# Performance work log

Measured on AMD Instinct MI355X. Metric: run time of the kernel, lower is better.

Reference implementation:

```python
import jax, jax.numpy as jnp
import numpy as np

WH, WW = 7, 7
N = WH * WW
DIM = 384
HEADS = 12
NW = 64          # windows per image
B_ = 2048        # batch * NW


def _relative_position_index():
    ch, cw = np.meshgrid(np.arange(WH), np.arange(WW), indexing='ij')
    coords = np.stack([ch, cw]).reshape(2, -1)                      # [2, N]
    rel = coords[:, :, None] - coords[:, None, :]                   # [2, N, N]
    rel = rel.transpose(1, 2, 0)
    rel[:, :, 0] += WH - 1
    rel[:, :, 1] += WW - 1
    rel[:, :, 0] *= 2 * WW - 1
    return jnp.asarray(rel.sum(-1), dtype=jnp.int32)                # [N, N]


def setup_inputs() -> dict:
    key = jax.random.key(0)
    ks = jax.random.split(key, 7)
    return {
        'x': jax.random.normal(ks[0], (B_, N, DIM), dtype=jnp.float32),
        'qkv_w': jax.random.normal(ks[1], (3 * DIM, DIM), dtype=jnp.float32) * 0.02,
        'qkv_b': jax.random.normal(ks[2], (3 * DIM,), dtype=jnp.float32) * 0.02,
        'proj_w': jax.random.normal(ks[3], (DIM, DIM), dtype=jnp.float32) * 0.02,
        'proj_b': jax.random.normal(ks[4], (DIM,), dtype=jnp.float32) * 0.02,
        'bias_table': jax.random.normal(ks[5], ((2 * WH - 1) * (2 * WW - 1), HEADS), dtype=jnp.float32) * 0.02,
        'mask': jax.random.normal(ks[6], (NW, N, N), dtype=jnp.float32),
        'rel_idx': _relative_position_index(),
    }


def reference(x, qkv_w, qkv_b, proj_w, proj_b, bias_table, mask, rel_idx):
    B_, n, C = x.shape
    H = HEADS
    hd = C // H
    scale = hd ** (-0.5)

    qkv = x @ qkv_w.T + qkv_b                                        # [B_, N, 3C]
    qkv = qkv.reshape(B_, n, 3, H, hd).transpose(2, 0, 3, 1, 4)      # [3, B_, H, N, hd]
    q, k, v = qkv[0], qkv[1], qkv[2]

    attn = jnp.einsum('bhqd,bhkd->bhqk', q * scale, k)               # [B_, H, N, N]

    rpb = bias_table[rel_idx.reshape(-1)].reshape(n, n, H)           # gather [N, N, H]
    attn = attn + rpb.transpose(2, 0, 1)[None]                       # [B_, H, N, N]

    nW = mask.shape[0]
    attn = attn.reshape(B_ // nW, nW, H, n, n) + mask[None, :, None]
    attn = attn.reshape(B_, H, n, n)
    attn = jax.nn.softmax(attn, axis=-1)

    out = jnp.einsum('bhqk,bhkd->bhqd', attn, v)                     # [B_, H, N, hd]
    out = out.transpose(0, 2, 1, 3).reshape(B_, n, C)
    return out @ proj_w.T + proj_b
```

## Files before the change

kernel.cpp:

```cpp
#include <hip/hip_runtime.h>
#include <hip/hip_bf16.h>
#include <cstdint>
#include <cstddef>

#define NTOK 49
#define DIM 384
#define HEADS 12
#define HD 32
#define NWIN 64
#define BATCH 2048
#define MROWS (BATCH * NTOK)

typedef unsigned short u16;
typedef __bf16 bf16x8 __attribute__((ext_vector_type(8)));
typedef unsigned short u16x8 __attribute__((ext_vector_type(8)));
typedef float f32x4 __attribute__((ext_vector_type(4)));

__device__ __forceinline__ u16 f2b(float f) {
  union { float f; unsigned u; } v; v.f = f;
  unsigned r = v.u + 0x7fffu + ((v.u >> 16) & 1u);
  return (u16)(r >> 16);
}

__device__ __forceinline__ bf16x8 ld_bf8(const u16* p) {
  u16x8 u = *(const u16x8*)p;
  return __builtin_bit_cast(bf16x8, u);
}

__device__ __forceinline__ void gload_lds16(const void* g, void* l) {
  __builtin_amdgcn_global_load_lds(
      (const __attribute__((address_space(1))) unsigned*)g,
      (__attribute__((address_space(3))) unsigned*)l, 16, 0, 0);
}

__global__ __launch_bounds__(256) void k_cast(const float* __restrict__ in,
                                              u16* __restrict__ out, int n4) {
  int i = blockIdx.x * 256 + threadIdx.x;
  if (i < n4) {
    float4 v = ((const float4*)in)[i];
    ushort4 o;
    o.x = f2b(v.x); o.y = f2b(v.y); o.z = f2b(v.z); o.w = f2b(v.w);
    ((ushort4*)out)[i] = o;
  }
}

__global__ __launch_bounds__(256) void k_rpbm(const float* __restrict__ bias_table,
                                              const float* __restrict__ mask,
                                              const int* __restrict__ rel_idx,
                                              float* __restrict__ out) {
  int idx = blockIdx.x * 256 + threadIdx.x;
  int r  = idx & 3;
  int l  = (idx >> 2) & 63;
  int ni = (idx >> 8) & 3;
  int mi = (idx >> 10) & 3;
  int w  = (idx >> 12) & 63;
  int h  = idx >> 18;
  int row = mi * 16 + (l >> 4) * 4 + r;
  int col = ni * 16 + (l & 15);
  float v = -1e30f;
  if (row < NTOK && col < NTOK)
    v = bias_table[rel_idx[row * NTOK + col] * HEADS + h] +
        mask[(w * NTOK + row) * NTOK + col];
  out[idx] = v;
}

template <int OUT_BF16>
__global__ __launch_bounds__(256) void k_gemm(const u16* __restrict__ A,
                                              const u16* __restrict__ B,
                                              const float* __restrict__ bias,
                                              void* __restrict__ Cv,
                                              int K, int N, int ntn, int grid_div8) {
  __shared__ u16 As[128 * 32];
  __shared__ u16 Bs[128 * 32];
  int bid = blockIdx.x;
  int tile = (bid & 7) * grid_div8 + (bid >> 3);
  int mt = tile / ntn, nt = tile % ntn;
  long m0 = (long)mt * 128;
  int n0 = nt * 128;
  int tid = threadIdx.x;
  int lane = tid & 63, wid = tid >> 6;
  int wr = (wid >> 1) * 64, wc = (wid & 1) * 64;
  int c = lane & 15, g = lane >> 4;

  int srow = wid * 16 + (lane >> 2);
  int scol = (lane & 3) * 8;
  const u16* gA = A + (m0 + srow) * (long)K + scol;
  const u16* gB = B + (long)(n0 + srow) * K + scol;
  u16* lA = &As[srow * 32 + scol];
  u16* lB = &Bs[srow * 32 + scol];

  f32x4 acc[4][4] = {};
  for (int kt = 0; kt < K; kt += 32) {
    __syncthreads();
    gload_lds16(gA + kt, lA);
    gload_lds16(gA + kt + 64L * K, lA + 64 * 32);
    gload_lds16(gB + kt, lB);
    gload_lds16(gB + kt + 64L * K, lB + 64 * 32);
    __syncthreads();
    bf16x8 af[4], bf_[4];
#pragma unroll
    for (int i = 0; i < 4; ++i) {
      af[i]  = ld_bf8(&As[(wr + i * 16 + c) * 32 + g * 8]);
      bf_[i] = ld_bf8(&Bs[(wc + i * 16 + c) * 32 + g * 8]);
    }
#pragma unroll
    for (int mi = 0; mi < 4; ++mi)
#pragma unroll
      for (int ni = 0; ni < 4; ++ni)
        acc[mi][ni] = __builtin_amdgcn_mfma_f32_16x16x32_bf16(
            af[mi], bf_[ni], acc[mi][ni], 0, 0, 0);
  }

#pragma unroll
  for (int mi = 0; mi < 4; ++mi)
#pragma unroll
    for (int ni = 0; ni < 4; ++ni) {
      int colg = n0 + wc + ni * 16 + c;
      float bv = bias[colg];
#pragma unroll
      for (int r = 0; r < 4; ++r) {
        long rowg = m0 + wr + mi * 16 + g * 4 + r;
        float val = acc[mi][ni][r] + bv;
        if (OUT_BF16)
          ((u16*)Cv)[rowg * N + colg] = f2b(val);
        else
          ((float*)Cv)[rowg * N + colg] = val;
      }
    }
}

__global__ __launch_bounds__(256) void k_attn(const u16* __restrict__ qkv,
                                              const float* __restrict__ rpbm,
                                              u16* __restrict__ attnout) {
  __shared__ u16 P_lds[4][64 * 64];
  __shared__ u16 vT_lds[4][32 * 64];
  int lane = threadIdx.x & 63, wid = threadIdx.x >> 6;
  int task = blockIdx.x * 4 + wid;
  int b = task / 12, h = task - b * 12;
  int w = b & 63;
  const u16* base = qkv + (size_t)b * (NTOK * 1152);
  int c = lane & 15, g = lane >> 4;

  u16* vt = vT_lds[wid];
  {
    const u16* vbase = base + 2 * DIM + h * HD;
#pragma unroll
    for (int t = 0; t < 4; ++t) {
      int idx = t * 64 + lane;
      int j = idx >> 2, d0 = (idx & 3) * 8;
      int jr = j < NTOK ? j : NTOK - 1;
      u16x8 vv = *(const u16x8*)(vbase + (size_t)jr * 1152 + d0);
#pragma unroll
      for (int dd = 0; dd < 8; ++dd) {
        int d = d0 + dd;
        int byte = (d * 128 + j * 2) ^ ((d & 7) << 4);
        *(u16*)((char*)vt + byte) = (u16)vv[dd];
      }
    }
  }

  bf16x8 qa[4], kb[4];
#pragma unroll
  for (int mi = 0; mi < 4; ++mi) {
    int row = mi * 16 + c; if (row > NTOK - 1) row = NTOK - 1;
    qa[mi] = ld_bf8(base + (size_t)row * 1152 + h * HD + g * 8);
  }
#pragma unroll
  for (int ni = 0; ni < 4; ++ni) {
    int row = ni * 16 + c; if (row > NTOK - 1) row = NTOK - 1;
    kb[ni] = ld_bf8(base + (size_t)row * 1152 + DIM + h * HD + g * 8);
  }

  f32x4 s[4][4] = {};
#pragma unroll
  for (int mi = 0; mi < 4; ++mi)
#pragma unroll
    for (int ni = 0; ni < 4; ++ni)
      s[mi][ni] = __builtin_amdgcn_mfma_f32_16x16x32_bf16(qa[mi], kb[ni],
                                                          s[mi][ni], 0, 0, 0);

  const float scale = 0.17677669529663687f;
  const f32x4* rp = (const f32x4*)(rpbm + ((size_t)(h * 64 + w)) * 4096);
#pragma unroll
  for (int mi = 0; mi < 4; ++mi)
#pragma unroll
    for (int ni = 0; ni < 4; ++ni) {
      f32x4 rv = rp[(mi * 4 + ni) * 64 + lane];
#pragma unroll
      for (int r = 0; r < 4; ++r)
        s[mi][ni][r] = s[mi][ni][r] * scale + rv[r];
    }

#pragma unroll
  for (int mi = 0; mi < 4; ++mi)
#pragma unroll
    for (int r = 0; r < 4; ++r) {
      float mx = fmaxf(fmaxf(s[mi][0][r], s[mi][1][r]),
                       fmaxf(s[mi][2][r], s[mi][3][r]));
      mx = fmaxf(mx, __shfl_xor(mx, 1));
      mx = fmaxf(mx, __shfl_xor(mx, 2));
      mx = fmaxf(mx, __shfl_xor(mx, 4));
      mx = fmaxf(mx, __shfl_xor(mx, 8));
      float sum = 0.f;
#pragma unroll
      for (int ni = 0; ni < 4; ++ni) {
        float p = __expf(s[mi][ni][r] - mx);
        s[mi][ni][r] = p;
        sum += p;
      }
      sum += __shfl_xor(sum, 1);
      sum += __shfl_xor(sum, 2);
      sum += __shfl_xor(sum, 4);
      sum += __shfl_xor(sum, 8);
      float inv = __builtin_amdgcn_rcpf(sum);
#pragma unroll
      for (int ni = 0; ni < 4; ++ni) s[mi][ni][r] *= inv;
    }

  u16* pl = P_lds[wid];
#pragma unroll
  for (int mi = 0; mi < 4; ++mi)
#pragma unroll
    for (int ni = 0; ni < 4; ++ni) {
      int col = ni * 16 + c;
#pragma unroll
      for (int r = 0; r < 4; ++r) {
        int row = mi * 16 + g * 4 + r;
        int byte = (row * 128 + col * 2) ^ ((row & 7) << 4);
        *(u16*)((char*)pl + byte) = f2b(s[mi][ni][r]);
      }
    }
  asm volatile("s_waitcnt lgkmcnt(0)" ::: "memory");

  f32x4 o[4][2] = {};
#pragma unroll
  for (int ks = 0; ks < 2; ++ks) {
    bf16x8 vb[2];
#pragma unroll
    for (int n2 = 0; n2 < 2; ++n2) {
      int d = n2 * 16 + c;
      int byte = (d * 128 + ks * 64 + g * 16) ^ ((d & 7) << 4);
      vb[n2] = __builtin_bit_cast(bf16x8, *(const u16x8*)((const char*)vt + byte));
    }
#pragma unroll
    for (int mi = 0; mi < 4; ++mi) {
      int row = mi * 16 + c;
      int byte = (row * 128 + ks * 64 + g * 16) ^ ((row & 7) << 4);
      bf16x8 pa = __builtin_bit_cast(bf16x8, *(const u16x8*)((const char*)pl + byte));
#pragma unroll
      for (int n2 = 0; n2 < 2; ++n2)
        o[mi][n2] = __builtin_amdgcn_mfma_f32_16x16x32_bf16(pa, vb[n2],
                                                            o[mi][n2], 0, 0, 0);
    }
  }

  u16* obase = attnout + (size_t)b * (NTOK * DIM) + h * HD;
#pragma unroll
  for (int mi = 0; mi < 4; ++mi)
#pragma unroll
    for (int r = 0; r < 4; ++r) {
      int row = mi * 16 + g * 4 + r;
      if (row < NTOK) {
#pragma unroll
        for (int n2 = 0; n2 < 2; ++n2)
          obase[(size_t)row * DIM + n2 * 16 + c] = f2b(o[mi][n2][r]);
      }
    }
}

extern "C" void kernel_launch(void* const* d_in, const int* in_sizes, int n_in,
                              void* d_out, int out_size, void* d_ws, size_t ws_size,
                              hipStream_t stream) {
  const float* x       = (const float*)d_in[0];
  const float* qkv_w   = (const float*)d_in[1];
  const float* qkv_b   = (const float*)d_in[2];
  const float* proj_w  = (const float*)d_in[3];
  const float* proj_b  = (const float*)d_in[4];
  const float* bias_tb = (const float*)d_in[5];
  const float* mask    = (const float*)d_in[6];
  const int*   rel_idx = (const int*)d_in[7];
  float* out = (float*)d_out;

  char* ws = (char*)d_ws;
  u16*   xb      = (u16*)(ws + 0);
  u16*   wqkvb   = (u16*)(ws + 77070336);
  u16*   wprojb  = (u16*)(ws + 77955072);
  float* rpbm    = (float*)(ws + 78249984);
  u16*   qkv     = (u16*)(ws + 90832896);
  u16*   attnout = (u16*)(ws + 322043904);

  k_cast<<<37632, 256, 0, stream>>>(x, xb, MROWS * DIM / 4);
  k_cast<<<432, 256, 0, stream>>>(qkv_w, wqkvb, 3 * DIM * DIM / 4);
  k_cast<<<144, 256, 0, stream>>>(proj_w, wprojb, DIM * DIM / 4);

  k_rpbm<<<12288, 256, 0, stream>>>(bias_tb, mask, rel_idx, rpbm);

  k_gemm<1><<<7056, 256, 0, stream>>>(xb, wqkvb, qkv_b, qkv, DIM, 3 * DIM, 9, 882);

  k_attn<<<6144, 256, 0, stream>>>(qkv, rpbm, attnout);

  k_gemm<0><<<2352, 256, 0, stream>>>(attnout, wprojb, proj_b, out, DIM, DIM, 3, 294);

  (void)in_sizes; (void)n_in; (void)out_size; (void)ws_size;
}
```

Measured before the change: 381.8 us.

## Fuse x cast into QKV GEMM, double-buffer GEMM, stage epilogue via LDS

```diff
diff --git a/kernel.cpp b/kernel.cpp
--- a/kernel.cpp
+++ b/kernel.cpp
@@ -5,9 +5,9 @@
 
 #define NTOK 49
 #define DIM 384
+#define KDIM 384
 #define HEADS 12
 #define HD 32
-#define NWIN 64
 #define BATCH 2048
 #define MROWS (BATCH * NTOK)
 
@@ -64,17 +64,15 @@
   out[idx] = v;
 }
 
-template <int OUT_BF16>
-__global__ __launch_bounds__(256) void k_gemm(const u16* __restrict__ A,
+template <int OUT_BF16, int A_F32, int NCOLS, int NTN, int GD8>
+__global__ __launch_bounds__(256) void k_gemm(const void* __restrict__ Av,
                                               const u16* __restrict__ B,
                                               const float* __restrict__ bias,
-                                              void* __restrict__ Cv,
-                                              int K, int N, int ntn, int grid_div8) {
-  __shared__ u16 As[128 * 32];
-  __shared__ u16 Bs[128 * 32];
+                                              void* __restrict__ Cv) {
+  __shared__ u16 sh[16384];
   int bid = blockIdx.x;
-  int tile = (bid & 7) * grid_div8 + (bid >> 3);
-  int mt = tile / ntn, nt = tile % ntn;
+  int tile = (bid & 7) * GD8 + (bid >> 3);
+  int mt = tile / NTN, nt = tile - mt * NTN;
   long m0 = (long)mt * 128;
   int n0 = nt * 128;
   int tid = threadIdx.x;
@@ -84,49 +82,121 @@
 
   int srow = wid * 16 + (lane >> 2);
   int scol = (lane & 3) * 8;
-  const u16* gA = A + (m0 + srow) * (long)K + scol;
-  const u16* gB = B + (long)(n0 + srow) * K + scol;
-  u16* lA = &As[srow * 32 + scol];
-  u16* lB = &Bs[srow * 32 + scol];
+  const u16* gB = B + (long)(n0 + srow) * KDIM + scol;
+
+  const u16* gA16 = nullptr;
+  const float* gAf = nullptr;
+  float4 areg[4];
+  int arow = tid >> 3;
+  int acol = (tid & 7) * 4;
+  if (A_F32) {
+    gAf = (const float*)Av + (m0 + arow) * KDIM + acol;
+#pragma unroll
+    for (int rp = 0; rp < 4; ++rp)
+      areg[rp] = *(const float4*)(gAf + rp * 32 * KDIM);
+  } else {
+    gA16 = (const u16*)Av + (m0 + srow) * (long)KDIM + scol;
+  }
 
   f32x4 acc[4][4] = {};
-  for (int kt = 0; kt < K; kt += 32) {
-    __syncthreads();
-    gload_lds16(gA + kt, lA);
-    gload_lds16(gA + kt + 64L * K, lA + 64 * 32);
-    gload_lds16(gB + kt, lB);
-    gload_lds16(gB + kt + 64L * K, lB + 64 * 32);
-    __syncthreads();
-    bf16x8 af[4], bf_[4];
+
+  auto STAGE = [&](int buf, int ktS) {
+    u16* As = sh + buf * 8192;
+    u16* Bs = As + 4096;
+    if (A_F32) {
+#pragma unroll
+      for (int rp = 0; rp < 4; ++rp) {
+        float4 v = areg[rp];
+        ushort4 o; o.x = f2b(v.x); o.y = f2b(v.y); o.z = f2b(v.z); o.w = f2b(v.w);
+        *(ushort4*)&As[(rp * 32 + arow) * 32 + acol] = o;
+      }
+      if (ktS + 32 < KDIM) {
+#pragma unroll
+        for (int rp = 0; rp < 4; ++rp)
+          areg[rp] = *(const float4*)(gAf + rp * 32 * KDIM + (ktS + 32));
+      }
+    } else {
+      gload_lds16(gA16 + ktS, &((u16*)As)[srow * 32 + scol]);
+      gload_lds16(gA16 + ktS + 64L * KDIM, &((u16*)As)[(srow + 64) * 32 + scol]);
+    }
+    gload_lds16(gB + ktS, &Bs[srow * 32 + scol]);
+    gload_lds16(gB + ktS + 64L * KDIM, &Bs[(srow + 64) * 32 + scol]);
+  };
+
+  STAGE(0, 0);
+  __syncthreads();
+  int cur = 0;
+  for (int kt = 0; kt < KDIM; kt += 32) {
+    if (kt + 32 < KDIM) STAGE(cur ^ 1, kt + 32);
+    const u16* As = sh + cur * 8192;
+    const u16* Bs = As + 4096;
+    bf16x8 af[4], bfr[4];
 #pragma unroll
     for (int i = 0; i < 4; ++i) {
       af[i]  = ld_bf8(&As[(wr + i * 16 + c) * 32 + g * 8]);
-      bf_[i] = ld_bf8(&Bs[(wc + i * 16 + c) * 32 + g * 8]);
+      bfr[i] = ld_bf8(&Bs[(wc + i * 16 + c) * 32 + g * 8]);
     }
 #pragma unroll
     for (int mi = 0; mi < 4; ++mi)
 #pragma unroll
       for (int ni = 0; ni < 4; ++ni)
         acc[mi][ni] = __builtin_amdgcn_mfma_f32_16x16x32_bf16(
-            af[mi], bf_[ni], acc[mi][ni], 0, 0, 0);
-  }
-
-#pragma unroll
-  for (int mi = 0; mi < 4; ++mi)
-#pragma unroll
-    for (int ni = 0; ni < 4; ++ni) {
-      int colg = n0 + wc + ni * 16 + c;
-      float bv = bias[colg];
-#pragma unroll
-      for (int r = 0; r < 4; ++r) {
-        long rowg = m0 + wr + mi * 16 + g * 4 + r;
-        float val = acc[mi][ni][r] + bv;
-        if (OUT_BF16)
-          ((u16*)Cv)[rowg * N + colg] = f2b(val);
-        else
-          ((float*)Cv)[rowg * N + colg] = val;
-      }
-    }
+            af[mi], bfr[ni], acc[mi][ni], 0, 0, 0);
+    __syncthreads();
+    cur ^= 1;
+  }
+
+  if (OUT_BF16) {
+    u16* C = (u16*)Cv;
+#pragma unroll
+    for (int mi = 0; mi < 4; ++mi)
+#pragma unroll
+      for (int ni = 0; ni < 4; ++ni) {
+        int col = wc + ni * 16 + c;
+        float bv = bias[n0 + col];
+#pragma unroll
+        for (int r = 0; r < 4; ++r) {
+          int row = wr + mi * 16 + g * 4 + r;
+          sh[row * 128 + col] = f2b(acc[mi][ni][r] + bv);
+        }
+      }
+    __syncthreads();
+#pragma unroll
+    for (int rep = 0; rep < 8; ++rep) {
+      int idx = rep * 2048 + tid * 8;
+      int row = idx >> 7, col = idx & 127;
+      *(u16x8*)(C + (m0 + row) * NCOLS + n0 + col) = *(const u16x8*)&sh[idx];
+    }
+  } else {
+    float* C = (float*)Cv;
+    float* shf = (float*)sh;
+#pragma unroll
+    for (int chunk = 0; chunk < 2; ++chunk) {
+      __syncthreads();
+      if ((wr >> 6) == chunk) {
+#pragma unroll
+        for (int mi = 0; mi < 4; ++mi)
+#pragma unroll
+          for (int ni = 0; ni < 4; ++ni) {
+            int col = wc + ni * 16 + c;
+            float bv = bias[n0 + col];
+#pragma unroll
+            for (int r = 0; r < 4; ++r) {
+              int lrow = mi * 16 + g * 4 + r;
+              shf[lrow * 128 + col] = acc[mi][ni][r] + bv;
+            }
+          }
+      }
+      __syncthreads();
+#pragma unroll
+      for (int rep = 0; rep < 8; ++rep) {
+        int idx = rep * 1024 + tid * 4;
+        int row = idx >> 7, col = idx & 127;
+        *(float4*)(C + (m0 + chunk * 64 + row) * NCOLS + n0 + col) =
+            *(const float4*)&shf[idx];
+      }
+    }
+  }
 }
 
 __global__ __launch_bounds__(256) void k_attn(const u16* __restrict__ qkv,
@@ -135,9 +205,13 @@
   __shared__ u16 P_lds[4][64 * 64];
   __shared__ u16 vT_lds[4][32 * 64];
   int lane = threadIdx.x & 63, wid = threadIdx.x >> 6;
-  int task = blockIdx.x * 4 + wid;
-  int b = task / 12, h = task - b * 12;
-  int w = b & 63;
+  int blk = blockIdx.x;
+  int w = blk / 96;
+  int rr = blk - w * 96;
+  int j = rr / 3;
+  int hb = rr - j * 3;
+  int b = j * 64 + w;
+  int h = hb * 4 + wid;
   const u16* base = qkv + (size_t)b * (NTOK * 1152);
   int c = lane & 15, g = lane >> 4;
 
@@ -147,13 +221,13 @@
 #pragma unroll
     for (int t = 0; t < 4; ++t) {
       int idx = t * 64 + lane;
-      int j = idx >> 2, d0 = (idx & 3) * 8;
-      int jr = j < NTOK ? j : NTOK - 1;
+      int jj = idx >> 2, d0 = (idx & 3) * 8;
+      int jr = jj < NTOK ? jj : NTOK - 1;
       u16x8 vv = *(const u16x8*)(vbase + (size_t)jr * 1152 + d0);
 #pragma unroll
       for (int dd = 0; dd < 8; ++dd) {
         int d = d0 + dd;
-        int byte = (d * 128 + j * 2) ^ ((d & 7) << 4);
+        int byte = (d * 128 + jj * 2) ^ ((d & 7) << 4);
         *(u16*)((char*)vt + byte) = (u16)vv[dd];
       }
     }
@@ -282,24 +356,24 @@
   float* out = (float*)d_out;
 
   char* ws = (char*)d_ws;
-  u16*   xb      = (u16*)(ws + 0);
-  u16*   wqkvb   = (u16*)(ws + 77070336);
-  u16*   wprojb  = (u16*)(ws + 77955072);
-  float* rpbm    = (float*)(ws + 78249984);
-  u16*   qkv     = (u16*)(ws + 90832896);
-  u16*   attnout = (u16*)(ws + 322043904);
-
-  k_cast<<<37632, 256, 0, stream>>>(x, xb, MROWS * DIM / 4);
+  u16*   wqkvb   = (u16*)(ws + 0);
+  u16*   wprojb  = (u16*)(ws + 884736);
+  float* rpbm    = (float*)(ws + 1179648);
+  u16*   qkv     = (u16*)(ws + 13762560);
+  u16*   attnout = (u16*)(ws + 244973568);
+
   k_cast<<<432, 256, 0, stream>>>(qkv_w, wqkvb, 3 * DIM * DIM / 4);
   k_cast<<<144, 256, 0, stream>>>(proj_w, wprojb, DIM * DIM / 4);
 
   k_rpbm<<<12288, 256, 0, stream>>>(bias_tb, mask, rel_idx, rpbm);
 
-  k_gemm<1><<<7056, 256, 0, stream>>>(xb, wqkvb, qkv_b, qkv, DIM, 3 * DIM, 9, 882);
+  k_gemm<1, 1, 1152, 9, 882><<<7056, 256, 0, stream>>>(
+      (const void*)x, wqkvb, qkv_b, (void*)qkv);
 
   k_attn<<<6144, 256, 0, stream>>>(qkv, rpbm, attnout);
 
-  k_gemm<0><<<2352, 256, 0, stream>>>(attnout, wprojb, proj_b, out, DIM, DIM, 3, 294);
+  k_gemm<0, 0, 384, 3, 294><<<2352, 256, 0, stream>>>(
+      (const void*)attnout, wprojb, proj_b, (void*)out);
 
   (void)in_sizes; (void)n_in; (void)out_size; (void)ws_size;
 }
```

Result: no change. 377.1 us (-1.2%).

## Fuse QKV projection, window attention and output projection into one per-window kernel

Applied to the files above, without the earlier changes.

```diff
diff --git a/kernel.cpp b/kernel.cpp
--- a/kernel.cpp
+++ b/kernel.cpp
@@ -7,9 +7,7 @@
 #define DIM 384
 #define HEADS 12
 #define HD 32
-#define NWIN 64
 #define BATCH 2048
-#define MROWS (BATCH * NTOK)
 
 typedef unsigned short u16;
 typedef __bf16 bf16x8 __attribute__((ext_vector_type(8)));
@@ -27,245 +25,276 @@
   return __builtin_bit_cast(bf16x8, u);
 }
 
-__device__ __forceinline__ void gload_lds16(const void* g, void* l) {
-  __builtin_amdgcn_global_load_lds(
-      (const __attribute__((address_space(1))) unsigned*)g,
-      (__attribute__((address_space(3))) unsigned*)l, 16, 0, 0);
-}
-
-__global__ __launch_bounds__(256) void k_cast(const float* __restrict__ in,
-                                              u16* __restrict__ out, int n4) {
-  int i = blockIdx.x * 256 + threadIdx.x;
-  if (i < n4) {
+#define MFMA16(a, b, cacc) __builtin_amdgcn_mfma_f32_16x16x32_bf16(a, b, cacc, 0, 0, 0)
+
+__global__ __launch_bounds__(256) void k_prep(const float* __restrict__ qkv_w,
+                                              u16* __restrict__ wqkvb,
+                                              const float* __restrict__ proj_w,
+                                              u16* __restrict__ wprojb,
+                                              const float* __restrict__ bias_table,
+                                              const float* __restrict__ mask,
+                                              const int* __restrict__ rel_idx,
+                                              float* __restrict__ rpbm) {
+  int blk = blockIdx.x;
+  if (blk < 576) {
+    const float* in;
+    u16* out;
+    int i;
+    if (blk < 432) { in = qkv_w; out = wqkvb; i = blk * 256 + threadIdx.x; }
+    else           { in = proj_w; out = wprojb; i = (blk - 432) * 256 + threadIdx.x; }
     float4 v = ((const float4*)in)[i];
     ushort4 o;
     o.x = f2b(v.x); o.y = f2b(v.y); o.z = f2b(v.z); o.w = f2b(v.w);
     ((ushort4*)out)[i] = o;
+  } else {
+    int idx = (blk - 576) * 256 + threadIdx.x;
+    int r  = idx & 3;
+    int l  = (idx >> 2) & 63;
+    int ni = (idx >> 8) & 3;
+    int mi = (idx >> 10) & 3;
+    int w  = (idx >> 12) & 63;
+    int h  = idx >> 18;
+    int row = mi * 16 + (l >> 4) * 4 + r;
+    int col = ni * 16 + (l & 15);
+    float v = -1e30f;
+    if (row < NTOK && col < NTOK)
+      v = bias_table[rel_idx[row * NTOK + col] * HEADS + h] +
+          mask[(w * NTOK + row) * NTOK + col];
+    rpbm[idx] = v;
   }
 }
 
-__global__ __launch_bounds__(256) void k_rpbm(const float* __restrict__ bias_table,
-                                              const float* __restrict__ mask,
-                                              const int* __restrict__ rel_idx,
-                                              float* __restrict__ out) {
-  int idx = blockIdx.x * 256 + threadIdx.x;
-  int r  = idx & 3;
-  int l  = (idx >> 2) & 63;
-  int ni = (idx >> 8) & 3;
-  int mi = (idx >> 10) & 3;
-  int w  = (idx >> 12) & 63;
-  int h  = idx >> 18;
-  int row = mi * 16 + (l >> 4) * 4 + r;
-  int col = ni * 16 + (l & 15);
-  float v = -1e30f;
-  if (row < NTOK && col < NTOK)
-    v = bias_table[rel_idx[row * NTOK + col] * HEADS + h] +
-        mask[(w * NTOK + row) * NTOK + col];
-  out[idx] = v;
-}
-
-template <int OUT_BF16>
-__global__ __launch_bounds__(256) void k_gemm(const u16* __restrict__ A,
-                                              const u16* __restrict__ B,
-                                              const float* __restrict__ bias,
-                                              void* __restrict__ Cv,
-                                              int K, int N, int ntn, int grid_div8) {
-  __shared__ u16 As[128 * 32];
-  __shared__ u16 Bs[128 * 32];
-  int bid = blockIdx.x;
-  int tile = (bid & 7) * grid_div8 + (bid >> 3);
-  int mt = tile / ntn, nt = tile % ntn;
-  long m0 = (long)mt * 128;
-  int n0 = nt * 128;
-  int tid = threadIdx.x;
-  int lane = tid & 63, wid = tid >> 6;
-  int wr = (wid >> 1) * 64, wc = (wid & 1) * 64;
-  int c = lane & 15, g = lane >> 4;
-
-  int srow = wid * 16 + (lane >> 2);
-  int scol = (lane & 3) * 8;
-  const u16* gA = A + (m0 + srow) * (long)K + scol;
-  const u16* gB = B + (long)(n0 + srow) * K + scol;
-  u16* lA = &As[srow * 32 + scol];
-  u16* lB = &Bs[srow * 32 + scol];
-
-  f32x4 acc[4][4] = {};
-  for (int kt = 0; kt < K; kt += 32) {
-    __syncthreads();
-    gload_lds16(gA + kt, lA);
-    gload_lds16(gA + kt + 64L * K, lA + 64 * 32);
-    gload_lds16(gB + kt, lB);
-    gload_lds16(gB + kt + 64L * K, lB + 64 * 32);
-    __syncthreads();
-    bf16x8 af[4], bf_[4];
-#pragma unroll
-    for (int i = 0; i < 4; ++i) {
-      af[i]  = ld_bf8(&As[(wr + i * 16 + c) * 32 + g * 8]);
-      bf_[i] = ld_bf8(&Bs[(wc + i * 16 + c) * 32 + g * 8]);
-    }
+__global__ __launch_bounds__(256, 1) void k_fused(const float* __restrict__ x,
+                                                  const u16* __restrict__ wqkv,
+                                                  const float* __restrict__ qkv_b,
+                                                  const u16* __restrict__ wproj,
+                                                  const float* __restrict__ proj_b,
+                                                  const float* __restrict__ rpbm,
+                                                  float* __restrict__ out) {
+  __shared__ __attribute__((aligned(16))) char lds[161792];
+  const int b = blockIdx.x;
+  const int w = b & 63;
+  const int tid = threadIdx.x;
+  const int lane = tid & 63, wid = tid >> 6;
+  const int c = lane & 15, g = lane >> 4;
+  char* xs = lds;
+  char* Ob = lds + 50176;
+  char* wv = lds + 100352 + wid * 15360;
+
+  {
+    const float4* xp = (const float4*)(x + (size_t)b * (NTOK * DIM));
+    for (int i = tid; i < 4704; i += 256) {
+      float4 v = xp[i];
+      int row = i / 96, col4 = i - row * 96;
+      ushort4 o;
+      o.x = f2b(v.x); o.y = f2b(v.y); o.z = f2b(v.z); o.w = f2b(v.w);
+      *(ushort4*)(xs + row * 784 + col4 * 8) = o;
+    }
+    uint4 z = {0, 0, 0, 0};
+    for (int t = tid; t < 735; t += 256)
+      *(uint4*)(xs + 38416 + t * 16) = z;
+  }
+  __syncthreads();
+
+  const float scale = 0.17677669529663687f;
+
+#define LOAD_AB(af, bf, kt, ABASE, ASTRIDE, BPTR)                               \
+  _Pragma("unroll") for (int mi = 0; mi < 4; ++mi)                              \
+      af[mi] = ld_bf8((const u16*)((ABASE) + (mi * 16 + c) * (ASTRIDE)) +       \
+                      (kt) * 32 + g * 8);                                       \
+  _Pragma("unroll") for (int nj = 0; nj < 6; ++nj)                              \
+      bf[nj] = ld_bf8(BPTR[nj] + (kt) * 32);
+
+#define MFMA_46(af, bf, ACC)                                                    \
+  _Pragma("unroll") for (int mi = 0; mi < 4; ++mi)                              \
+  _Pragma("unroll") for (int nj = 0; nj < 6; ++nj)                              \
+      ACC[mi][nj] = MFMA16(af[mi], bf[nj], ACC[mi][nj]);
+
+  for (int hh = 0; hh < 3; ++hh) {
+    const int h = wid * 3 + hh;
+
+    int ncol[6];
+    ncol[0] = h * 32;        ncol[1] = h * 32 + 16;
+    ncol[2] = 384 + h * 32;  ncol[3] = 384 + h * 32 + 16;
+    ncol[4] = 768 + h * 32;  ncol[5] = 768 + h * 32 + 16;
+    const u16* bp[6];
+#pragma unroll
+    for (int nj = 0; nj < 6; ++nj)
+      bp[nj] = wqkv + (size_t)(ncol[nj] + c) * 384 + g * 8;
+
+    f32x4 acc[4][6] = {};
+    {
+      bf16x8 afA[4], bfA[6], afB[4], bfB[6];
+      LOAD_AB(afA, bfA, 0, xs, 784, bp);
+#pragma unroll
+      for (int kt = 0; kt < 12; kt += 2) {
+        if (kt + 1 < 12) { LOAD_AB(afB, bfB, kt + 1, xs, 784, bp); }
+        MFMA_46(afA, bfA, acc);
+        if (kt + 2 < 12) { LOAD_AB(afA, bfA, kt + 2, xs, 784, bp); }
+        MFMA_46(afB, bfB, acc);
+      }
+    }
+
+    asm volatile("s_waitcnt lgkmcnt(0)" ::: "memory");
+    __builtin_amdgcn_sched_barrier(0);
+
+#pragma unroll
+    for (int nj = 0; nj < 6; ++nj) {
+      float bv = qkv_b[ncol[nj] + c];
+      int d = (nj & 1) * 16 + c;
+#pragma unroll
+      for (int mi = 0; mi < 4; ++mi) {
+#pragma unroll
+        for (int r = 0; r < 4; ++r) {
+          int tok = mi * 16 + g * 4 + r;
+          float v = acc[mi][nj][r] + bv;
+          if (nj < 2)
+            *(u16*)(wv + tok * 80 + d * 2) = f2b(v * scale);
+          else if (nj < 4)
+            *(u16*)(wv + 5120 + tok * 80 + d * 2) = f2b(v);
+          else
+            *(u16*)(wv + 10240 + d * 144 + tok * 2) = f2b(v);
+        }
+      }
+    }
+    asm volatile("s_waitcnt lgkmcnt(0)" ::: "memory");
+    __builtin_amdgcn_sched_barrier(0);
+
+    f32x4 s[4][4];
+    {
+      bf16x8 qf[4], kf[4];
+#pragma unroll
+      for (int i = 0; i < 4; ++i) {
+        qf[i] = ld_bf8((const u16*)(wv + (i * 16 + c) * 80) + g * 8);
+        kf[i] = ld_bf8((const u16*)(wv + 5120 + (i * 16 + c) * 80) + g * 8);
+      }
+      f32x4 zf = {0.f, 0.f, 0.f, 0.f};
+#pragma unroll
+      for (int mi = 0; mi < 4; ++mi)
+#pragma unroll
+        for (int nj = 0; nj < 4; ++nj)
+          s[mi][nj] = MFMA16(qf[mi], kf[nj], zf);
+    }
+
+    const f32x4* rp = (const f32x4*)(rpbm + ((size_t)(h * 64 + w)) * 4096);
 #pragma unroll
     for (int mi = 0; mi < 4; ++mi)
 #pragma unroll
-      for (int ni = 0; ni < 4; ++ni)
-        acc[mi][ni] = __builtin_amdgcn_mfma_f32_16x16x32_bf16(
-            af[mi], bf_[ni], acc[mi][ni], 0, 0, 0);
+      for (int nj = 0; nj < 4; ++nj) {
+        f32x4 rv = rp[(mi * 4 + nj) * 64 + lane];
+#pragma unroll
+        for (int r = 0; r < 4; ++r) s[mi][nj][r] += rv[r];
+      }
+
+#pragma unroll
+    for (int mi = 0; mi < 4; ++mi)
+#pragma unroll
+      for (int r = 0; r < 4; ++r) {
+        float mx = fmaxf(fmaxf(s[mi][0][r], s[mi][1][r]),
+                         fmaxf(s[mi][2][r], s[mi][3][r]));
+        mx = fmaxf(mx, __shfl_xor(mx, 1));
+        mx = fmaxf(mx, __shfl_xor(mx, 2));
+        mx = fmaxf(mx, __shfl_xor(mx, 4));
+        mx = fmaxf(mx, __shfl_xor(mx, 8));
+        float sum = 0.f;
+#pragma unroll
+        for (int nj = 0; nj < 4; ++nj) {
+          float p = __expf(s[mi][nj][r] - mx);
+          s[mi][nj][r] = p;
+          sum += p;
+        }
+        sum += __shfl_xor(sum, 1);
+        sum += __shfl_xor(sum, 2);
+        sum += __shfl_xor(sum, 4);
+        sum += __shfl_xor(sum, 8);
+        float inv = __builtin_amdgcn_rcpf(sum);
+#pragma unroll
+        for (int nj = 0; nj < 4; ++nj) s[mi][nj][r] *= inv;
+      }
+
+#pragma unroll
+    for (int mi = 0; mi < 4; ++mi)
+#pragma unroll
+      for (int nj = 0; nj < 4; ++nj) {
+        int col = nj * 16 + c;
+#pragma unroll
+        for (int r = 0; r < 4; ++r) {
+          int tok = mi * 16 + g * 4 + r;
+          *(u16*)(wv + tok * 144 + col * 2) = f2b(s[mi][nj][r]);
+        }
+      }
+    asm volatile("s_waitcnt lgkmcnt(0)" ::: "memory");
+    __builtin_amdgcn_sched_barrier(0);
+
+    f32x4 o[4][2] = {};
+#pragma unroll
+    for (int ks = 0; ks < 2; ++ks) {
+      bf16x8 vf[2];
+#pragma unroll
+      for (int n2 = 0; n2 < 2; ++n2)
+        vf[n2] = ld_bf8((const u16*)(wv + 10240 + (n2 * 16 + c) * 144) +
+                        ks * 32 + g * 8);
+#pragma unroll
+      for (int mi = 0; mi < 4; ++mi) {
+        bf16x8 pa = ld_bf8((const u16*)(wv + (mi * 16 + c) * 144) + ks * 32 + g * 8);
+#pragma unroll
+        for (int n2 = 0; n2 < 2; ++n2)
+          o[mi][n2] = MFMA16(pa, vf[n2], o[mi][n2]);
+      }
+    }
+
+#pragma unroll
+    for (int mi = 0; mi < 4; ++mi)
+#pragma unroll
+      for (int n2 = 0; n2 < 2; ++n2) {
+        int ocol = h * 32 + n2 * 16 + c;
+#pragma unroll
+        for (int r = 0; r < 4; ++r) {
+          int tok = mi * 16 + g * 4 + r;
+          *(u16*)(Ob + tok * 784 + ocol * 2) = f2b(o[mi][n2][r]);
+        }
+      }
   }
 
-#pragma unroll
-  for (int mi = 0; mi < 4; ++mi)
-#pragma unroll
-    for (int ni = 0; ni < 4; ++ni) {
-      int colg = n0 + wc + ni * 16 + c;
-      float bv = bias[colg];
-#pragma unroll
-      for (int r = 0; r < 4; ++r) {
-        long rowg = m0 + wr + mi * 16 + g * 4 + r;
-        float val = acc[mi][ni][r] + bv;
-        if (OUT_BF16)
-          ((u16*)Cv)[rowg * N + colg] = f2b(val);
-        else
-          ((float*)Cv)[rowg * N + colg] = val;
-      }
-    }
-}
-
-__global__ __launch_bounds__(256) void k_attn(const u16* __restrict__ qkv,
-                                              const float* __restrict__ rpbm,
-                                              u16* __restrict__ attnout) {
-  __shared__ u16 P_lds[4][64 * 64];
-  __shared__ u16 vT_lds[4][32 * 64];
-  int lane = threadIdx.x & 63, wid = threadIdx.x >> 6;
-  int task = blockIdx.x * 4 + wid;
-  int b = task / 12, h = task - b * 12;
-  int w = b & 63;
-  const u16* base = qkv + (size_t)b * (NTOK * 1152);
-  int c = lane & 15, g = lane >> 4;
-
-  u16* vt = vT_lds[wid];
+  __syncthreads();
+
   {
-    const u16* vbase = base + 2 * DIM + h * HD;
-#pragma unroll
-    for (int t = 0; t < 4; ++t) {
-      int idx = t * 64 + lane;
-      int j = idx >> 2, d0 = (idx & 3) * 8;
-      int jr = j < NTOK ? j : NTOK - 1;
-      u16x8 vv = *(const u16x8*)(vbase + (size_t)jr * 1152 + d0);
-#pragma unroll
-      for (int dd = 0; dd < 8; ++dd) {
-        int d = d0 + dd;
-        int byte = (d * 128 + j * 2) ^ ((d & 7) << 4);
-        *(u16*)((char*)vt + byte) = (u16)vv[dd];
+    const int oc0 = wid * 96;
+    const u16* pp[6];
+#pragma unroll
+    for (int nj = 0; nj < 6; ++nj)
+      pp[nj] = wproj + (size_t)(oc0 + nj * 16 + c) * 384 + g * 8;
+
+    f32x4 ap[4][6] = {};
+    {
+      bf16x8 afA[4], bfA[6], afB[4], bfB[6];
+      LOAD_AB(afA, bfA, 0, Ob, 784, pp);
+#pragma unroll
+      for (int kt = 0; kt < 12; kt += 2) {
+        if (kt + 1 < 12) { LOAD_AB(afB, bfB, kt + 1, Ob, 784, pp); }
+        MFMA_46(afA, bfA, ap);
+        if (kt + 2 < 12) { LOAD_AB(afA, bfA, kt + 2, Ob, 784, pp); }
+        MFMA_46(afB, bfB, ap);
+      }
+    }
+
+#pragma unroll
+    for (int nj = 0; nj < 6; ++nj) {
+      float bv = proj_b[oc0 + nj * 16 + c];
+#pragma unroll
+      for (int mi = 0; mi < 4; ++mi) {
+#pragma unroll
+        for (int r = 0; r < 4; ++r) {
+          int tok = mi * 16 + g * 4 + r;
+          if (tok < NTOK)
+            out[((size_t)b * NTOK + tok) * 384 + oc0 + nj * 16 + c] =
+                ap[mi][nj][r] + bv;
+        }
       }
     }
   }
-
-  bf16x8 qa[4], kb[4];
-#pragma unroll
-  for (int mi = 0; mi < 4; ++mi) {
-    int row = mi * 16 + c; if (row > NTOK - 1) row = NTOK - 1;
-    qa[mi] = ld_bf8(base + (size_t)row * 1152 + h * HD + g * 8);
-  }
-#pragma unroll
-  for (int ni = 0; ni < 4; ++ni) {
-    int row = ni * 16 + c; if (row > NTOK - 1) row = NTOK - 1;
-    kb[ni] = ld_bf8(base + (size_t)row * 1152 + DIM + h * HD + g * 8);
-  }
-
-  f32x4 s[4][4] = {};
-#pragma unroll
-  for (int mi = 0; mi < 4; ++mi)
-#pragma unroll
-    for (int ni = 0; ni < 4; ++ni)
-      s[mi][ni] = __builtin_amdgcn_mfma_f32_16x16x32_bf16(qa[mi], kb[ni],
-                                                          s[mi][ni], 0, 0, 0);
-
-  const float scale = 0.17677669529663687f;
-  const f32x4* rp = (const f32x4*)(rpbm + ((size_t)(h * 64 + w)) * 4096);
-#pragma unroll
-  for (int mi = 0; mi < 4; ++mi)
-#pragma unroll
-    for (int ni = 0; ni < 4; ++ni) {
-      f32x4 rv = rp[(mi * 4 + ni) * 64 + lane];
-#pragma unroll
-      for (int r = 0; r < 4; ++r)
-        s[mi][ni][r] = s[mi][ni][r] * scale + rv[r];
-    }
-
-#pragma unroll
-  for (int mi = 0; mi < 4; ++mi)
-#pragma unroll
-    for (int r = 0; r < 4; ++r) {
-      float mx = fmaxf(fmaxf(s[mi][0][r], s[mi][1][r]),
-                       fmaxf(s[mi][2][r], s[mi][3][r]));
-      mx = fmaxf(mx, __shfl_xor(mx, 1));
-      mx = fmaxf(mx, __shfl_xor(mx, 2));
-      mx = fmaxf(mx, __shfl_xor(mx, 4));
-      mx = fmaxf(mx, __shfl_xor(mx, 8));
-      float sum = 0.f;
-#pragma unroll
-      for (int ni = 0; ni < 4; ++ni) {
-        float p = __expf(s[mi][ni][r] - mx);
-        s[mi][ni][r] = p;
-        sum += p;
-      }
-      sum += __shfl_xor(sum, 1);
-      sum += __shfl_xor(sum, 2);
-      sum += __shfl_xor(sum, 4);
-      sum += __shfl_xor(sum, 8);
-      float inv = __builtin_amdgcn_rcpf(sum);
-#pragma unroll
-      for (int ni = 0; ni < 4; ++ni) s[mi][ni][r] *= inv;
-    }
-
-  u16* pl = P_lds[wid];
-#pragma unroll
-  for (int mi = 0; mi < 4; ++mi)
-#pragma unroll
-    for (int ni = 0; ni < 4; ++ni) {
-      int col = ni * 16 + c;
-#pragma unroll
-      for (int r = 0; r < 4; ++r) {
-        int row = mi * 16 + g * 4 + r;
-        int byte = (row * 128 + col * 2) ^ ((row & 7) << 4);
-        *(u16*)((char*)pl + byte) = f2b(s[mi][ni][r]);
-      }
-    }
-  asm volatile("s_waitcnt lgkmcnt(0)" ::: "memory");
-
-  f32x4 o[4][2] = {};
-#pragma unroll
-  for (int ks = 0; ks < 2; ++ks) {
-    bf16x8 vb[2];
-#pragma unroll
-    for (int n2 = 0; n2 < 2; ++n2) {
-      int d = n2 * 16 + c;
-      int byte = (d * 128 + ks * 64 + g * 16) ^ ((d & 7) << 4);
-      vb[n2] = __builtin_bit_cast(bf16x8, *(const u16x8*)((const char*)vt + byte));
-    }
-#pragma unroll
-    for (int mi = 0; mi < 4; ++mi) {
-      int row = mi * 16 + c;
-      int byte = (row * 128 + ks * 64 + g * 16) ^ ((row & 7) << 4);
-      bf16x8 pa = __builtin_bit_cast(bf16x8, *(const u16x8*)((const char*)pl + byte));
-#pragma unroll
-      for (int n2 = 0; n2 < 2; ++n2)
-        o[mi][n2] = __builtin_amdgcn_mfma_f32_16x16x32_bf16(pa, vb[n2],
-                                                            o[mi][n2], 0, 0, 0);
-    }
-  }
-
-  u16* obase = attnout + (size_t)b * (NTOK * DIM) + h * HD;
-#pragma unroll
-  for (int mi = 0; mi < 4; ++mi)
-#pragma unroll
-    for (int r = 0; r < 4; ++r) {
-      int row = mi * 16 + g * 4 + r;
-      if (row < NTOK) {
-#pragma unroll
-        for (int n2 = 0; n2 < 2; ++n2)
-          obase[(size_t)row * DIM + n2 * 16 + c] = f2b(o[mi][n2][r]);
-      }
-    }
+#undef LOAD_AB
+#undef MFMA_46
 }
 
 extern "C" void kernel_launch(void* const* d_in, const int* in_sizes, int n_in,
@@ -282,24 +311,14 @@
   float* out = (float*)d_out;
 
   char* ws = (char*)d_ws;
-  u16*   xb      = (u16*)(ws + 0);
-  u16*   wqkvb   = (u16*)(ws + 77070336);
-  u16*   wprojb  = (u16*)(ws + 77955072);
-  float* rpbm    = (float*)(ws + 78249984);
-  u16*   qkv     = (u16*)(ws + 90832896);
-  u16*   attnout = (u16*)(ws + 322043904);
-
-  k_cast<<<37632, 256, 0, stream>>>(x, xb, MROWS * DIM / 4);
-  k_cast<<<432, 256, 0, stream>>>(qkv_w, wqkvb, 3 * DIM * DIM / 4);
-  k_cast<<<144, 256, 0, stream>>>(proj_w, wprojb, DIM * DIM / 4);
-
-  k_rpbm<<<12288, 256, 0, stream>>>(bias_tb, mask, rel_idx, rpbm);
-
-  k_gemm<1><<<7056, 256, 0, stream>>>(xb, wqkvb, qkv_b, qkv, DIM, 3 * DIM, 9, 882);
-
-  k_attn<<<6144, 256, 0, stream>>>(qkv, rpbm, attnout);
-
-  k_gemm<0><<<2352, 256, 0, stream>>>(attnout, wprojb, proj_b, out, DIM, DIM, 3, 294);
+  u16*   wqkvb  = (u16*)(ws + 0);
+  u16*   wprojb = (u16*)(ws + 884736);
+  float* rpbm   = (float*)(ws + 1179648);
+
+  k_prep<<<12864, 256, 0, stream>>>(qkv_w, wqkvb, proj_w, wprojb,
+                                    bias_tb, mask, rel_idx, rpbm);
+
+  k_fused<<<BATCH, 256, 0, stream>>>(x, wqkvb, qkv_b, wprojb, proj_b, rpbm, out);
 
   (void)in_sizes; (void)n_in; (void)out_size; (void)ws_size;
 }
```

Result: slower. 526.6 us (+37.9%).
